# Performance work log

Measured on AMD Instinct MI355X. Metric: run time of the kernel, lower is better.

## Reference

```python
import jax, jax.numpy as jnp
import numpy as np
from jax import lax

DIM = 256
RATE = 4
MAX_SK_IT = 10
N = RATE
NC = N * DIM            # 1024
NG = N * N + 2 * N      # 24


def setup_inputs() -> dict:
    key = jax.random.key(0)
    ks = jax.random.split(key, 5)
    h = jax.random.normal(ks[0], (8, 4096, N, DIM), jnp.float32)
    norm_weight = jax.random.normal(ks[1], (NC,), jnp.float32)
    w = jax.random.normal(ks[2], (NC, NG), jnp.float32) * 0.02
    alpha = jax.random.normal(ks[3], (3,), jnp.float32) * 0.01
    beta = jax.random.normal(ks[4], (NG,), jnp.float32) * 0.1
    return {"h": h, "norm_weight": norm_weight, "w": w, "alpha": alpha, "beta": beta}


def _sinkhorn(K, iters):
    # Sinkhorn-Knopp diagonal scalings u, v such that diag(u) @ K @ diag(v)
    # is (approximately) doubly stochastic. K: (BL, N, N) positive.
    BL, n, _ = K.shape
    u = jnp.ones((BL, n), K.dtype)
    v = jnp.ones((BL, n), K.dtype)

    def body(carry, _):
        u, v = carry
        u = 1.0 / (jnp.einsum('bij,bj->bi', K, v) + 1e-8)
        v = 1.0 / (jnp.einsum('bij,bi->bj', K, u) + 1e-8)
        return (u, v), None

    (u, v), _ = lax.scan(body, (u, v), None, length=iters)
    return u, v


def reference(h, norm_weight, w, alpha, beta):
    B, L, n, D = h.shape
    hf = h.reshape(B, L, n * D)              # (B,L,NC)
    hv = norm_weight * hf                    # mapping uses raw norm weight
    H = hv @ w                               # (B,L,NG)
    r = jnp.linalg.norm(hf, axis=-1, keepdims=True) / np.float32(np.sqrt(n * D))
    r_ = 1.0 / (r + 1e-6)

    H_pre = jax.nn.sigmoid(r_ * H[..., :n] * alpha[0] + beta[:n])            # (B,L,N)
    H_post = 2.0 * jax.nn.sigmoid(r_ * H[..., n:2 * n] * alpha[1] + beta[n:2 * n])
    H_res = (r_ * H[..., 2 * n:] * alpha[2] + beta[2 * n:]).reshape(B, L, n, n)

    K = jnp.exp(H_res).reshape(B * L, n, n)
    u, v = _sinkhorn(K, MAX_SK_IT)
    u = lax.stop_gradient(u)
    v = lax.stop_gradient(v)
    P = (u[:, :, None] * K * v[:, None, :]).reshape(B, L, n, n)

    # process
    h_pre = jnp.einsum('bln,blnd->bld', H_pre, h)[:, :, None, :]  # (B,L,1,D)
    h_res = jnp.einsum('blnm,blmd->blnd', P, h)                   # (B,L,N,D)

    # depth_connection with h_out = h_pre (identity inner layer)
    out = H_post[..., None] * h_pre + h_res                       # (B,L,N,D)
    return out
```

## Files before the change

kernel.cpp:

```cpp
#include <hip/hip_runtime.h>
#include <math.h>


#define NTOK 16

typedef __attribute__((ext_vector_type(2))) _Float16 h2v;

__device__ __forceinline__ float fdot2f(unsigned int a, unsigned int b, float c) {
#if __has_builtin(__builtin_amdgcn_fdot2)
    return __builtin_amdgcn_fdot2(__builtin_bit_cast(h2v, a),
                                  __builtin_bit_cast(h2v, b), c, false);
#else
    h2v av = __builtin_bit_cast(h2v, a);
    h2v bv = __builtin_bit_cast(h2v, b);
    return fmaf((float)av[1], (float)bv[1],
           fmaf((float)av[0], (float)bv[0], c));
#endif
}

__device__ __forceinline__ unsigned int pk_f16(float a, float b) {
    const auto p = __builtin_amdgcn_cvt_pkrtz(a, b);
    return __builtin_bit_cast(unsigned int, p);
}

__device__ __forceinline__ float sigmoid_f(float z) {
    return 1.0f / (1.0f + __expf(-z));
}

__device__ __forceinline__ float row16_sum(float x) {
    x += __int_as_float(__builtin_amdgcn_update_dpp(
        0, __float_as_int(x), 0x121, 0xf, 0xf, false));
    x += __int_as_float(__builtin_amdgcn_update_dpp(
        0, __float_as_int(x), 0x122, 0xf, 0xf, false));
    x += __int_as_float(__builtin_amdgcn_update_dpp(
        0, __float_as_int(x), 0x124, 0xf, 0xf, false));
    x += __int_as_float(__builtin_amdgcn_update_dpp(
        0, __float_as_int(x), 0x128, 0xf, 0xf, false));
    return x;
}

__global__ __launch_bounds__(256)
void prep_kernel(const float* __restrict__ nw,
                 const float* __restrict__ w,
                 const float* __restrict__ alpha,
                 unsigned short* __restrict__ wt)
{
    const int tid = blockIdx.x * 256 + threadIdx.x;
    const int flat = 4 * tid;
    const float4 w4 = *(const float4*)(w + flat);
    const float a0 = alpha[0], a1 = alpha[1], a2 = alpha[2];
    const float vals[4] = {w4.x, w4.y, w4.z, w4.w};
    #pragma unroll
    for (int c = 0; c < 4; ++c) {
        const int f = flat + c;
        const int k = f / 24;
        const int n = f - 24 * k;
        const float as = (n < 4) ? a0 : ((n < 8) ? a1 : a2);
        const unsigned int p = pk_f16(as * nw[k] * vals[c], 0.f);
        wt[n * 1024 + k] = (unsigned short)(p & 0xffffu);
    }
}

__global__ __launch_bounds__(256)
void mhc_kernel(const float* __restrict__ h,
                const unsigned short* __restrict__ wt,
                const float* __restrict__ beta,
                float* __restrict__ out)
{
    const int tid  = threadIdx.x;
    const int lane = tid & 63;
    const int wv   = tid >> 6;
    const int ksl  = lane & 15;
    const int ng   = lane >> 4;

    __shared__ float Hpart[NTOK][28];
    __shared__ float smalls[NTOK][26];

    const long tok0 = (long)blockIdx.x * NTOK;
    const int t0 = 4 * wv;
    const float* ph = h + (tok0 + t0) * 1024 + 4 * ksl;
    const uint2* twp = (const uint2*)wt + (6 * ng) * 256 + ksl;

    float acc[4][6], r2[4];
    #pragma unroll
    for (int t = 0; t < 4; ++t) {
        r2[t] = 0.f;
        #pragma unroll
        for (int j = 0; j < 6; ++j) acc[t][j] = 0.f;
    }

    #pragma unroll 1
    for (int e = 0; e < 16; ++e) {
        float4 xf[4];
        #pragma unroll
        for (int t = 0; t < 4; ++t)
            xf[t] = *(const float4*)(ph + t * 1024 + 64 * e);
        uint2 wr[6];
        #pragma unroll
        for (int j = 0; j < 6; ++j) wr[j] = twp[j * 256 + e * 16];

        uint2 xw[4];
        #pragma unroll
        for (int t = 0; t < 4; ++t) {
            xw[t].x = pk_f16(xf[t].x, xf[t].y);
            xw[t].y = pk_f16(xf[t].z, xf[t].w);
        }

        #pragma unroll
        for (int j = 0; j < 6; ++j) {
            #pragma unroll
            for (int t = 0; t < 4; ++t) {
                acc[t][j] = fdot2f(xw[t].y, wr[j].y,
                            fdot2f(xw[t].x, wr[j].x, acc[t][j]));
            }
        }
        #pragma unroll
        for (int t = 0; t < 4; ++t) {
            r2[t] = fmaf(xf[t].w, xf[t].w, fmaf(xf[t].z, xf[t].z,
                    fmaf(xf[t].y, xf[t].y, fmaf(xf[t].x, xf[t].x, r2[t]))));
        }
    }

    #pragma unroll
    for (int t = 0; t < 4; ++t) {
        #pragma unroll
        for (int j = 0; j < 6; ++j) acc[t][j] = row16_sum(acc[t][j]);
        r2[t] = row16_sum(r2[t]);
    }
    if (ksl == 0) {
        #pragma unroll
        for (int t = 0; t < 4; ++t) {
            #pragma unroll
            for (int j = 0; j < 6; ++j)
                Hpart[t0 + t][6 * ng + j] = acc[t][j];
            if (ng == 0) Hpart[t0 + t][24] = r2[t];
        }
    }
    __syncthreads();

    if (tid < NTOK) {
        const int t = tid;
        float Hp[24];
        #pragma unroll
        for (int q = 0; q < 24; ++q) Hp[q] = Hpart[t][q];
        const float r2v = Hpart[t][24];
        const float r_ = 1.0f / (sqrtf(r2v) * 0.03125f + 1e-6f);

        float Hpre[4], Hpost[4], K[16];
        #pragma unroll
        for (int n = 0; n < 4; ++n)
            Hpre[n] = sigmoid_f(fmaf(r_, Hp[n], beta[n]));
        #pragma unroll
        for (int n = 0; n < 4; ++n)
            Hpost[n] = 2.0f * sigmoid_f(fmaf(r_, Hp[4 + n], beta[4 + n]));
        #pragma unroll
        for (int q = 0; q < 16; ++q)
            K[q] = __expf(fmaf(r_, Hp[8 + q], beta[8 + q]));

        float u0=1.f,u1=1.f,u2=1.f,u3=1.f;
        float v0=1.f,v1=1.f,v2=1.f,v3=1.f;
        for (int itr = 0; itr < 10; ++itr) {
            u0 = 1.0f/(K[0]*v0  + K[1]*v1  + K[2]*v2  + K[3]*v3  + 1e-8f);
            u1 = 1.0f/(K[4]*v0  + K[5]*v1  + K[6]*v2  + K[7]*v3  + 1e-8f);
            u2 = 1.0f/(K[8]*v0  + K[9]*v1  + K[10]*v2 + K[11]*v3 + 1e-8f);
            u3 = 1.0f/(K[12]*v0 + K[13]*v1 + K[14]*v2 + K[15]*v3 + 1e-8f);
            v0 = 1.0f/(K[0]*u0  + K[4]*u1  + K[8]*u2  + K[12]*u3 + 1e-8f);
            v1 = 1.0f/(K[1]*u0  + K[5]*u1  + K[9]*u2  + K[13]*u3 + 1e-8f);
            v2 = 1.0f/(K[2]*u0  + K[6]*u1  + K[10]*u2 + K[14]*u3 + 1e-8f);
            v3 = 1.0f/(K[3]*u0  + K[7]*u1  + K[11]*u2 + K[15]*u3 + 1e-8f);
        }
        smalls[t][0] = Hpre[0];  smalls[t][1] = Hpre[1];
        smalls[t][2] = Hpre[2];  smalls[t][3] = Hpre[3];
        smalls[t][4] = Hpost[0]; smalls[t][5] = Hpost[1];
        smalls[t][6] = Hpost[2]; smalls[t][7] = Hpost[3];
        smalls[t][8]  = u0*K[0]*v0;   smalls[t][9]  = u0*K[1]*v1;
        smalls[t][10] = u0*K[2]*v2;   smalls[t][11] = u0*K[3]*v3;
        smalls[t][12] = u1*K[4]*v0;   smalls[t][13] = u1*K[5]*v1;
        smalls[t][14] = u1*K[6]*v2;   smalls[t][15] = u1*K[7]*v3;
        smalls[t][16] = u2*K[8]*v0;   smalls[t][17] = u2*K[9]*v1;
        smalls[t][18] = u2*K[10]*v2;  smalls[t][19] = u2*K[11]*v3;
        smalls[t][20] = u3*K[12]*v0;  smalls[t][21] = u3*K[13]*v1;
        smalls[t][22] = u3*K[14]*v2;  smalls[t][23] = u3*K[15]*v3;
    }
    __syncthreads();

    const int gg = wv;
    const float* p0 = h + tok0 * 1024 + 4 * lane;
    float4 ca0, ca1, ca2, ca3, cb0, cb1, cb2, cb3;
    {
        ca0 = *(const float4*)(p0);       ca1 = *(const float4*)(p0 + 256);
        ca2 = *(const float4*)(p0 + 512); ca3 = *(const float4*)(p0 + 768);
        const float* q = p0 + 1024;
        cb0 = *(const float4*)(q);        cb1 = *(const float4*)(q + 256);
        cb2 = *(const float4*)(q + 512);  cb3 = *(const float4*)(q + 768);
    }
    for (int it = 0; it < NTOK; ++it) {
        const long tok = tok0 + it;
        const float4 xm0 = ca0, xm1 = ca1, xm2 = ca2, xm3 = ca3;
        ca0 = cb0; ca1 = cb1; ca2 = cb2; ca3 = cb3;
        if (it + 2 < NTOK) {
            const float* p = p0 + (it + 2) * 1024;
            cb0 = *(const float4*)(p);       cb1 = *(const float4*)(p + 256);
            cb2 = *(const float4*)(p + 512); cb3 = *(const float4*)(p + 768);
        }
        const float hp0 = smalls[it][0], hp1 = smalls[it][1];
        const float hp2 = smalls[it][2], hp3 = smalls[it][3];
        const float hpost = smalls[it][4 + gg];
        const float P0 = smalls[it][8 + 4*gg + 0];
        const float P1 = smalls[it][8 + 4*gg + 1];
        const float P2 = smalls[it][8 + 4*gg + 2];
        const float P3 = smalls[it][8 + 4*gg + 3];

        float4 o;
        {
            const float hpre = hp0*xm0.x + hp1*xm1.x + hp2*xm2.x + hp3*xm3.x;
            o.x = fmaf(hpost, hpre, P0*xm0.x + P1*xm1.x + P2*xm2.x + P3*xm3.x);
        }
        {
            const float hpre = hp0*xm0.y + hp1*xm1.y + hp2*xm2.y + hp3*xm3.y;
            o.y = fmaf(hpost, hpre, P0*xm0.y + P1*xm1.y + P2*xm2.y + P3*xm3.y);
        }
        {
            const float hpre = hp0*xm0.z + hp1*xm1.z + hp2*xm2.z + hp3*xm3.z;
            o.z = fmaf(hpost, hpre, P0*xm0.z + P1*xm1.z + P2*xm2.z + P3*xm3.z);
        }
        {
            const float hpre = hp0*xm0.w + hp1*xm1.w + hp2*xm2.w + hp3*xm3.w;
            o.w = fmaf(hpost, hpre, P0*xm0.w + P1*xm1.w + P2*xm2.w + P3*xm3.w);
        }
        *(float4*)(out + tok * 1024 + gg * 256 + 4 * lane) = o;
    }
}

extern "C" void kernel_launch(void* const* d_in, const int* in_sizes, int n_in,
                              void* d_out, int out_size, void* d_ws, size_t ws_size,
                              hipStream_t stream) {
    const float* h     = (const float*)d_in[0];
    const float* nw    = (const float*)d_in[1];
    const float* w     = (const float*)d_in[2];
    const float* alpha = (const float*)d_in[3];
    const float* beta  = (const float*)d_in[4];
    float* out = (float*)d_out;
    unsigned short* wt = (unsigned short*)d_ws;

    prep_kernel<<<24, 256, 0, stream>>>(nw, w, alpha, wt);
    mhc_kernel<<<2048, 256, 0, stream>>>(h, wt, beta, out);
}
```

Before: 82.48 us.

## Split fused kernel into scalar phase and mixing phase, stashing coefficients in output

Replaces the single fused kernel with two launches. The first computes the mapping GEMV, the norm and the Sinkhorn iterations per wave, using a wave-local LDS fence instead of block barriers. It writes the 24 per-token coefficients into the start of each token's output row. The second kernel reloads these coefficients and h to produce the output, overwriting the stash. This removes the two block-wide __syncthreads and the single-thread serial section, at the cost of a second full pass over h from memory and an extra launch.

```diff
diff --git a/kernel.cpp b/kernel.cpp
--- a/kernel.cpp
+++ b/kernel.cpp
@@ -1,8 +1,6 @@
 #include <hip/hip_runtime.h>
 #include <math.h>
 
-
-#define NTOK 16
 
 typedef __attribute__((ext_vector_type(2))) _Float16 h2v;
 
@@ -25,6 +23,11 @@
 
 __device__ __forceinline__ float sigmoid_f(float z) {
     return 1.0f / (1.0f + __expf(-z));
+}
+
+__device__ __forceinline__ void wave_lds_fence() {
+    asm volatile("s_waitcnt lgkmcnt(0)" ::: "memory");
+    __builtin_amdgcn_sched_barrier(0);
 }
 
 __device__ __forceinline__ float row16_sum(float x) {
@@ -62,10 +65,10 @@
 }
 
 __global__ __launch_bounds__(256)
-void mhc_kernel(const float* __restrict__ h,
-                const unsigned short* __restrict__ wt,
-                const float* __restrict__ beta,
-                float* __restrict__ out)
+void phaseA_kernel(const float* __restrict__ h,
+                   const unsigned short* __restrict__ wt,
+                   const float* __restrict__ beta,
+                   float* __restrict__ out)
 {
     const int tid  = threadIdx.x;
     const int lane = tid & 63;
@@ -73,10 +76,9 @@
     const int ksl  = lane & 15;
     const int ng   = lane >> 4;
 
-    __shared__ float Hpart[NTOK][28];
-    __shared__ float smalls[NTOK][26];
-
-    const long tok0 = (long)blockIdx.x * NTOK;
+    __shared__ float Hpart[16][28];
+
+    const long tok0 = (long)blockIdx.x * 16;
     const int t0 = 4 * wv;
     const float* ph = h + (tok0 + t0) * 1024 + 4 * ksl;
     const uint2* twp = (const uint2*)wt + (6 * ng) * 256 + ksl;
@@ -136,10 +138,10 @@
             if (ng == 0) Hpart[t0 + t][24] = r2[t];
         }
     }
-    __syncthreads();
-
-    if (tid < NTOK) {
-        const int t = tid;
+    wave_lds_fence();
+
+    if (lane < 4) {
+        const int t = t0 + lane;
         float Hp[24];
         #pragma unroll
         for (int q = 0; q < 24; ++q) Hp[q] = Hpart[t][q];
@@ -169,66 +171,75 @@
             v2 = 1.0f/(K[2]*u0  + K[6]*u1  + K[10]*u2 + K[14]*u3 + 1e-8f);
             v3 = 1.0f/(K[3]*u0  + K[7]*u1  + K[11]*u2 + K[15]*u3 + 1e-8f);
         }
-        smalls[t][0] = Hpre[0];  smalls[t][1] = Hpre[1];
-        smalls[t][2] = Hpre[2];  smalls[t][3] = Hpre[3];
-        smalls[t][4] = Hpost[0]; smalls[t][5] = Hpost[1];
-        smalls[t][6] = Hpost[2]; smalls[t][7] = Hpost[3];
-        smalls[t][8]  = u0*K[0]*v0;   smalls[t][9]  = u0*K[1]*v1;
-        smalls[t][10] = u0*K[2]*v2;   smalls[t][11] = u0*K[3]*v3;
-        smalls[t][12] = u1*K[4]*v0;   smalls[t][13] = u1*K[5]*v1;
-        smalls[t][14] = u1*K[6]*v2;   smalls[t][15] = u1*K[7]*v3;
-        smalls[t][16] = u2*K[8]*v0;   smalls[t][17] = u2*K[9]*v1;
-        smalls[t][18] = u2*K[10]*v2;  smalls[t][19] = u2*K[11]*v3;
-        smalls[t][20] = u3*K[12]*v0;  smalls[t][21] = u3*K[13]*v1;
-        smalls[t][22] = u3*K[14]*v2;  smalls[t][23] = u3*K[15]*v3;
-    }
-    __syncthreads();
-
-    const int gg = wv;
-    const float* p0 = h + tok0 * 1024 + 4 * lane;
-    float4 ca0, ca1, ca2, ca3, cb0, cb1, cb2, cb3;
-    {
-        ca0 = *(const float4*)(p0);       ca1 = *(const float4*)(p0 + 256);
-        ca2 = *(const float4*)(p0 + 512); ca3 = *(const float4*)(p0 + 768);
-        const float* q = p0 + 1024;
-        cb0 = *(const float4*)(q);        cb1 = *(const float4*)(q + 256);
-        cb2 = *(const float4*)(q + 512);  cb3 = *(const float4*)(q + 768);
-    }
-    for (int it = 0; it < NTOK; ++it) {
-        const long tok = tok0 + it;
-        const float4 xm0 = ca0, xm1 = ca1, xm2 = ca2, xm3 = ca3;
-        ca0 = cb0; ca1 = cb1; ca2 = cb2; ca3 = cb3;
-        if (it + 2 < NTOK) {
-            const float* p = p0 + (it + 2) * 1024;
-            cb0 = *(const float4*)(p);       cb1 = *(const float4*)(p + 256);
-            cb2 = *(const float4*)(p + 512); cb3 = *(const float4*)(p + 768);
-        }
-        const float hp0 = smalls[it][0], hp1 = smalls[it][1];
-        const float hp2 = smalls[it][2], hp3 = smalls[it][3];
-        const float hpost = smalls[it][4 + gg];
-        const float P0 = smalls[it][8 + 4*gg + 0];
-        const float P1 = smalls[it][8 + 4*gg + 1];
-        const float P2 = smalls[it][8 + 4*gg + 2];
-        const float P3 = smalls[it][8 + 4*gg + 3];
-
+        float4 o0, o1, o2, o3, o4, o5;
+        o0.x = Hpre[0];  o0.y = Hpre[1];  o0.z = Hpre[2];  o0.w = Hpre[3];
+        o1.x = Hpost[0]; o1.y = Hpost[1]; o1.z = Hpost[2]; o1.w = Hpost[3];
+        o2.x = u0*K[0]*v0;  o2.y = u0*K[1]*v1;  o2.z = u0*K[2]*v2;  o2.w = u0*K[3]*v3;
+        o3.x = u1*K[4]*v0;  o3.y = u1*K[5]*v1;  o3.z = u1*K[6]*v2;  o3.w = u1*K[7]*v3;
+        o4.x = u2*K[8]*v0;  o4.y = u2*K[9]*v1;  o4.z = u2*K[10]*v2; o4.w = u2*K[11]*v3;
+        o5.x = u3*K[12]*v0; o5.y = u3*K[13]*v1; o5.z = u3*K[14]*v2; o5.w = u3*K[15]*v3;
+        float* sp = out + (tok0 + t) * 1024;
+        *(float4*)(sp + 0)  = o0;  *(float4*)(sp + 4)  = o1;
+        *(float4*)(sp + 8)  = o2;  *(float4*)(sp + 12) = o3;
+        *(float4*)(sp + 16) = o4;  *(float4*)(sp + 20) = o5;
+    }
+}
+
+__global__ __launch_bounds__(256)
+void phaseC_kernel(const float* __restrict__ h,
+                   float* out)
+{
+    const int tid  = threadIdx.x;
+    const int lane = tid & 63;
+    const int wv   = tid >> 6;
+    const long gw  = (long)blockIdx.x * 4 + wv;
+
+    #pragma unroll 2
+    for (int i = 0; i < 4; ++i) {
+        const long tok = gw * 4 + i;
+
+        const float* sp = out + tok * 1024;
+        const float4 s0  = *(const float4*)(sp + 0);
+        const float4 s1  = *(const float4*)(sp + 4);
+        const float4 q0  = *(const float4*)(sp + 8);
+        const float4 q1  = *(const float4*)(sp + 12);
+        const float4 q2  = *(const float4*)(sp + 16);
+        const float4 q3  = *(const float4*)(sp + 20);
+
+        const float* pm = h + tok * 1024 + 4 * lane;
+        const float4 xm0 = *(const float4*)(pm);
+        const float4 xm1 = *(const float4*)(pm + 256);
+        const float4 xm2 = *(const float4*)(pm + 512);
+        const float4 xm3 = *(const float4*)(pm + 768);
+
+        float hpre[4];
+        hpre[0] = s0.x*xm0.x + s0.y*xm1.x + s0.z*xm2.x + s0.w*xm3.x;
+        hpre[1] = s0.x*xm0.y + s0.y*xm1.y + s0.z*xm2.y + s0.w*xm3.y;
+        hpre[2] = s0.x*xm0.z + s0.y*xm1.z + s0.z*xm2.z + s0.w*xm3.z;
+        hpre[3] = s0.x*xm0.w + s0.y*xm1.w + s0.z*xm2.w + s0.w*xm3.w;
+
+        float* po = out + tok * 1024 + 4 * lane;
         float4 o;
-        {
-            const float hpre = hp0*xm0.x + hp1*xm1.x + hp2*xm2.x + hp3*xm3.x;
-            o.x = fmaf(hpost, hpre, P0*xm0.x + P1*xm1.x + P2*xm2.x + P3*xm3.x);
-        }
-        {
-            const float hpre = hp0*xm0.y + hp1*xm1.y + hp2*xm2.y + hp3*xm3.y;
-            o.y = fmaf(hpost, hpre, P0*xm0.y + P1*xm1.y + P2*xm2.y + P3*xm3.y);
-        }
-        {
-            const float hpre = hp0*xm0.z + hp1*xm1.z + hp2*xm2.z + hp3*xm3.z;
-            o.z = fmaf(hpost, hpre, P0*xm0.z + P1*xm1.z + P2*xm2.z + P3*xm3.z);
-        }
-        {
-            const float hpre = hp0*xm0.w + hp1*xm1.w + hp2*xm2.w + hp3*xm3.w;
-            o.w = fmaf(hpost, hpre, P0*xm0.w + P1*xm1.w + P2*xm2.w + P3*xm3.w);
-        }
-        *(float4*)(out + tok * 1024 + gg * 256 + 4 * lane) = o;
+        o.x = fmaf(s1.x, hpre[0], q0.x*xm0.x + q0.y*xm1.x + q0.z*xm2.x + q0.w*xm3.x);
+        o.y = fmaf(s1.x, hpre[1], q0.x*xm0.y + q0.y*xm1.y + q0.z*xm2.y + q0.w*xm3.y);
+        o.z = fmaf(s1.x, hpre[2], q0.x*xm0.z + q0.y*xm1.z + q0.z*xm2.z + q0.w*xm3.z);
+        o.w = fmaf(s1.x, hpre[3], q0.x*xm0.w + q0.y*xm1.w + q0.z*xm2.w + q0.w*xm3.w);
+        *(float4*)(po) = o;
+        o.x = fmaf(s1.y, hpre[0], q1.x*xm0.x + q1.y*xm1.x + q1.z*xm2.x + q1.w*xm3.x);
+        o.y = fmaf(s1.y, hpre[1], q1.x*xm0.y + q1.y*xm1.y + q1.z*xm2.y + q1.w*xm3.y);
+        o.z = fmaf(s1.y, hpre[2], q1.x*xm0.z + q1.y*xm1.z + q1.z*xm2.z + q1.w*xm3.z);
+        o.w = fmaf(s1.y, hpre[3], q1.x*xm0.w + q1.y*xm1.w + q1.z*xm2.w + q1.w*xm3.w);
+        *(float4*)(po + 256) = o;
+        o.x = fmaf(s1.z, hpre[0], q2.x*xm0.x + q2.y*xm1.x + q2.z*xm2.x + q2.w*xm3.x);
+        o.y = fmaf(s1.z, hpre[1], q2.x*xm0.y + q2.y*xm1.y + q2.z*xm2.y + q2.w*xm3.y);
+        o.z = fmaf(s1.z, hpre[2], q2.x*xm0.z + q2.y*xm1.z + q2.z*xm2.z + q2.w*xm3.z);
+        o.w = fmaf(s1.z, hpre[3], q2.x*xm0.w + q2.y*xm1.w + q2.z*xm2.w + q2.w*xm3.w);
+        *(float4*)(po + 512) = o;
+        o.x = fmaf(s1.w, hpre[0], q3.x*xm0.x + q3.y*xm1.x + q3.z*xm2.x + q3.w*xm3.x);
+        o.y = fmaf(s1.w, hpre[1], q3.x*xm0.y + q3.y*xm1.y + q3.z*xm2.y + q3.w*xm3.y);
+        o.z = fmaf(s1.w, hpre[2], q3.x*xm0.z + q3.y*xm1.z + q3.z*xm2.z + q3.w*xm3.z);
+        o.w = fmaf(s1.w, hpre[3], q3.x*xm0.w + q3.y*xm1.w + q3.z*xm2.w + q3.w*xm3.w);
+        *(float4*)(po + 768) = o;
     }
 }
 
@@ -244,5 +255,6 @@
     unsigned short* wt = (unsigned short*)d_ws;
 
     prep_kernel<<<24, 256, 0, stream>>>(nw, w, alpha, wt);
-    mhc_kernel<<<2048, 256, 0, stream>>>(h, wt, beta, out);
-}
+    phaseA_kernel<<<2048, 256, 0, stream>>>(h, wt, beta, out);
+    phaseC_kernel<<<2048, 256, 0, stream>>>(h, out);
+}
```

Result: slower. 122.8 us (+48.9%).
